# Kernel tuning notes

Measured on AMD Instinct MI355X. Metric: run time of the kernel, lower is better.

The kernel has to match this reference:

```python
import jax, jax.numpy as jnp
import numpy as np

N_NODES = 50000
N_EDGES = 800000
NFEAT, NHID, NHEAD, NCLASS = 512, 64, 8, 40
NEG_SLOPE = 0.2  # LeakyReLU alpha from __init__


def setup_inputs() -> dict:
    key = jax.random.key(0)
    ks = jax.random.split(key, 8)
    glorot = lambda k, shape: jax.random.normal(k, shape, jnp.float32) * (2.0 / (shape[-2] + shape[-1])) ** 0.5
    return {
        "x": jax.random.normal(ks[0], (N_NODES, NFEAT), jnp.float32),
        "edge_list": jax.random.randint(ks[1], (2, N_EDGES), 0, N_NODES, jnp.int32),
        # nhead input-layer GATconv params: weight [H, nfeat, nhid], att [H, 2*nhid], bias [H, nhid]
        "W1": glorot(ks[2], (NHEAD, NFEAT, NHID)),
        "a1": jax.random.normal(ks[3], (NHEAD, 2 * NHID), jnp.float32) * 0.1,
        "b1": jnp.zeros((NHEAD, NHID), jnp.float32),
        # single output-head GATconv: [nhid*nhead, nclass]
        "W2": glorot(ks[4], (NHEAD * NHID, NCLASS)),
        "a2": jax.random.normal(ks[5], (2 * NCLASS,), jnp.float32) * 0.1,
        "b2": jnp.zeros((NCLASS,), jnp.float32),
    }


def _gat_layer(x, W, a, b, src, dst, n_nodes):
    """One GATconv head (eval mode, dropout = identity)."""
    h = x @ W                                  # [N, F]
    f = W.shape[-1]
    s_src = h @ a[:f]                          # [N] per-node src score
    s_dst = h @ a[f:]                          # [N] per-node dst score
    e = jax.nn.leaky_relu(s_src[src] + s_dst[dst], NEG_SLOPE)  # [E]
    # segment softmax over incoming edges of each dst node (numerically stable)
    m = jax.ops.segment_max(e, dst, num_segments=n_nodes)
    m = jax.lax.stop_gradient(jnp.where(jnp.isfinite(m), m, 0.0))
    w = jnp.exp(e - m[dst])
    denom = jax.ops.segment_sum(w, dst, num_segments=n_nodes)
    alpha = w / jnp.maximum(denom[dst], 1e-16)                 # [E]
    out = jax.ops.segment_sum(alpha[:, None] * h[src], dst, num_segments=n_nodes)
    return out + b


def reference(x, edge_list, W1, a1, b1, W2, a2, b2):
    n = x.shape[0]
    src, dst = edge_list[0], edge_list[1]
    # multi-head input layer, concat along feature dim
    heads = jax.vmap(lambda W, a, b: _gat_layer(x, W, a, b, src, dst, n))(W1, a1, b1)  # [H, N, nhid]
    h = jax.nn.elu(jnp.transpose(heads, (1, 0, 2)).reshape(n, -1))                      # [N, H*nhid]
    # single output head (mean over nhead_out=1)
    out = _gat_layer(h, W2, a2, b2, src, dst, n)                                        # [N, nclass]
    return jax.nn.log_softmax(out, axis=1)
```

## Files before the change

kernel.cpp:

```cpp
#include <hip/hip_runtime.h>
#include <math.h>

#define N_NODES 50000
#define N_EDGES 800000
#define NFEAT 512
#define NHID 64
#define NHEAD 8
#define NCLASS 40
#define NEG_SLOPE 0.2f

#define N_RT 3125
#define N_RT_PAD 3128
#define SCAN_NBLK 49
#define RT_BLK 4
#define ATT1_CHUNK 12500

typedef __attribute__((ext_vector_type(8))) short short8;
typedef __attribute__((ext_vector_type(4))) short short4v;
typedef __attribute__((ext_vector_type(4))) float f32x4;

__device__ __forceinline__ float bf2f(short s) {
    return __uint_as_float(((unsigned)(unsigned short)s) << 16);
}
__device__ __forceinline__ short f2bf(float f) {
    unsigned u = __float_as_uint(f);
    unsigned r = (u + 0x7FFFu + ((u >> 16) & 1u)) >> 16;
    return (short)(unsigned short)r;
}
__device__ __forceinline__ int swz(int s) { return s ^ ((s >> 4) & 7); }



__global__ void count_deg(const int* __restrict__ el, int* __restrict__ deg) {
    int e = blockIdx.x * blockDim.x + threadIdx.x;
    if (e < N_EDGES) atomicAdd(&deg[el[N_EDGES + e]], 1);
}

__global__ __launch_bounds__(256) void scan1(const int* __restrict__ deg,
                                             int* __restrict__ loc,
                                             int* __restrict__ bsum) {
    int tid = threadIdx.x, lane = tid & 63, w = tid >> 6;
    int base = blockIdx.x * 1024 + tid * 4;
    int d0 = (base + 0 < N_NODES) ? deg[base + 0] : 0;
    int d1 = (base + 1 < N_NODES) ? deg[base + 1] : 0;
    int d2 = (base + 2 < N_NODES) ? deg[base + 2] : 0;
    int d3 = (base + 3 < N_NODES) ? deg[base + 3] : 0;
    int s0 = d0, s1 = s0 + d1, s2 = s1 + d2, s3 = s2 + d3;
    int t = s3;
#pragma unroll
    for (int d = 1; d < 64; d <<= 1) {
        int u = __shfl_up(t, d);
        if (lane >= d) t += u;
    }
    __shared__ int wsum[4];
    if (lane == 63) wsum[w] = t;
    __syncthreads();
    int woff = 0;
#pragma unroll
    for (int j = 0; j < 4; ++j) woff += (j < w) ? wsum[j] : 0;
    int excl = woff + t - s3;
    if (base + 0 < N_NODES) loc[base + 0] = excl + s0;
    if (base + 1 < N_NODES) loc[base + 1] = excl + s1;
    if (base + 2 < N_NODES) loc[base + 2] = excl + s2;
    if (base + 3 < N_NODES) loc[base + 3] = excl + s3;
    if (tid == 255) bsum[blockIdx.x] = woff + t;
}

__global__ __launch_bounds__(256) void scan3(const int* __restrict__ deg,
                                             const int* __restrict__ loc,
                                             const int* __restrict__ bsum,
                                             int* __restrict__ ptr,
                                             int* __restrict__ cursor) {
    __shared__ int sOff;
    if (threadIdx.x < 64) {
        int lane = threadIdx.x;
        int v = (lane < SCAN_NBLK && lane < (int)blockIdx.x) ? bsum[lane] : 0;
#pragma unroll
        for (int m = 1; m < 64; m <<= 1) v += __shfl_xor(v, m);
        if (lane == 0) sOff = v;
    }
    __syncthreads();
    int off = sOff;
    int base = blockIdx.x * 1024 + threadIdx.x * 4;
    if (blockIdx.x == 0 && threadIdx.x == 0) ptr[0] = 0;
#pragma unroll
    for (int k = 0; k < 4; ++k) {
        int i = base + k;
        if (i < N_NODES) {
            int P = off + loc[i];
            ptr[i + 1] = P;
            cursor[i] = P - deg[i];
        }
    }
}

__global__ void scatter_k(const int* __restrict__ el, int* __restrict__ cursor,
                          int* __restrict__ esrc) {
    int e = blockIdx.x * blockDim.x + threadIdx.x;
    if (e >= N_EDGES) return;
    int dst = el[N_EDGES + e];
    int p = atomicAdd(&cursor[dst], 1);
    esrc[p] = el[e];
}

__global__ __launch_bounds__(256) void pack_w(const float* __restrict__ W1,
                                              const float* __restrict__ W2,
                                              const float* __restrict__ a1,
                                              short* __restrict__ Wp1a,
                                              short* __restrict__ Wp2) {
    int t = blockIdx.x * 256 + threadIdx.x;
    if (t < 36864) {
        int l = t & 63;
        int idx = t >> 6;
        int ct = idx % 9;
        int ksg = idx / 9;
        int ks = ksg & 15, g = ksg >> 4;
        short8 o;
        if (ct < 8) {
            int c = g * 128 + ct * 16 + (l & 15);
            int head = c >> 6, f = c & 63;
            int k0 = ks * 32 + (l >> 4) * 8;
#pragma unroll
            for (int j = 0; j < 8; ++j)
                o[j] = f2bf(W1[(size_t)head * NFEAT * NHID + (k0 + j) * NHID + f]);
        } else {
            int col = l & 15;
            int k0 = ks * 32 + (l >> 4) * 8;
#pragma unroll
            for (int j = 0; j < 8; ++j) o[j] = 0;
            if (col < 4) {
                int head = 2 * g + (col >> 1);
                const float* av = a1 + head * 128 + (col & 1) * 64;
                const float* wb = W1 + (size_t)head * NFEAT * NHID;
#pragma unroll
                for (int j = 0; j < 8; ++j) {
                    const float* wr = wb + (size_t)(k0 + j) * NHID;
                    float s = 0.f;
                    for (int f = 0; f < NHID; ++f) s += wr[f] * av[f];
                    o[j] = f2bf(s);
                }
            }
        }
        *(short8*)(Wp1a + (size_t)t * 8) = o;
    } else if (t < 36864 + 3072) {
        int u = t - 36864;
        int l = u & 63;
        int kc = u >> 6;
        int ct2 = kc % 3, ks = kc / 3;
        int col = ct2 * 16 + (l & 15);
        short8 o;
#pragma unroll
        for (int j = 0; j < 8; ++j) {
            int kp = ks * 32 + (l >> 4) * 8 + j;
            int head = kp >> 6, fp = kp & 63;
            int l15 = fp >> 2, ctp = fp & 3;
            int ct = ((head & 1) << 2) | ctp;
            int gg = head >> 1;
            int orig_k = gg * 128 + ct * 16 + l15;
            o[j] = (col < NCLASS) ? f2bf(W2[(size_t)orig_k * NCLASS + col]) : (short)0;
        }
        *(short8*)(Wp2 + (size_t)u * 8) = o;
    }
}

__global__ __launch_bounds__(256, 2) void gemm1(const float* __restrict__ x,
                                                const short* __restrict__ Wp1a,
                                                short* __restrict__ h1p,
                                                float* __restrict__ s1s,
                                                float* __restrict__ s1d) {
    __shared__ short As[RT_BLK * 16 * 64 * 8];
    int w = threadIdx.x >> 6, l = threadIdx.x & 63;
    int g = w;
    int rt0 = blockIdx.x * RT_BLK;
    int row0 = rt0 * 16;

#pragma unroll
    for (int u = 0; u < 4 * RT_BLK; ++u) {
        int idx = threadIdx.x + u * 256;
        int rl = idx >> 6, cg = idx & 63;
        int row = row0 + rl;
        short8 o;
        if (row < N_NODES) {
            const float* p = x + (size_t)row * NFEAT + cg * 8;
            f32x4 v0 = __builtin_nontemporal_load((const f32x4*)p);
            f32x4 v1 = __builtin_nontemporal_load((const f32x4*)(p + 4));
            o[0] = f2bf(v0[0]); o[1] = f2bf(v0[1]); o[2] = f2bf(v0[2]); o[3] = f2bf(v0[3]);
            o[4] = f2bf(v1[0]); o[5] = f2bf(v1[1]); o[6] = f2bf(v1[2]); o[7] = f2bf(v1[3]);
        } else {
#pragma unroll
            for (int j = 0; j < 8; ++j) o[j] = 0;
        }
        int rtl = rl >> 4, rloc = rl & 15, ks = cg >> 2, sub = cg & 3;
        int slot = (rtl * 16 + ks) * 64 + rloc + sub * 16;
        *(short8*)(As + swz(slot) * 8) = o;
    }
    __syncthreads();

    f32x4 acc[RT_BLK][9];
#pragma unroll
    for (int i = 0; i < RT_BLK; ++i)
#pragma unroll
        for (int ct = 0; ct < 9; ++ct) acc[i][ct] = (f32x4){0.f, 0.f, 0.f, 0.f};

    const short* bP = Wp1a + (size_t)g * (16 * 9 * 512) + l * 8;
#pragma unroll 2
    for (int ks = 0; ks < 16; ++ks) {
        short8 b[9];
#pragma unroll
        for (int ct = 0; ct < 9; ++ct) b[ct] = *(const short8*)(bP + ks * 4608 + ct * 512);
        short8 a[RT_BLK];
#pragma unroll
        for (int i = 0; i < RT_BLK; ++i)
            a[i] = *(const short8*)(As + swz((i * 16 + ks) * 64 + l) * 8);
#pragma unroll
        for (int i = 0; i < RT_BLK; ++i)
#pragma unroll
            for (int ct = 0; ct < 9; ++ct)
                acc[i][ct] = __builtin_amdgcn_mfma_f32_16x16x32_bf16(a[i], b[ct], acc[i][ct], 0, 0, 0);
    }

    int l15 = l & 15;
    int rbase = (l >> 4) * 4;
#pragma unroll
    for (int i = 0; i < RT_BLK; ++i)
#pragma unroll
        for (int r = 0; r < 4; ++r) {
            int row = (rt0 + i) * 16 + rbase + r;
            if (row < N_NODES) {
                short4v o0, o1;
#pragma unroll
                for (int c = 0; c < 4; ++c) { o0[c] = f2bf(acc[i][c][r]); o1[c] = f2bf(acc[i][4 + c][r]); }
                size_t base = (size_t)row * 512 + g * 128 + l15 * 4;
                *(short4v*)(h1p + base) = o0;
                *(short4v*)(h1p + base + 64) = o1;
                float sv = acc[i][8][r];
                if (l15 == 0)      s1s[row * 8 + 2 * g]     = sv;
                else if (l15 == 1) s1d[row * 8 + 2 * g]     = sv;
                else if (l15 == 2) s1s[row * 8 + 2 * g + 1] = sv;
                else if (l15 == 3) s1d[row * 8 + 2 * g + 1] = sv;
            }
        }
}

__global__ __launch_bounds__(256, 4) void att1(const int* __restrict__ ptr,
                                               const int* __restrict__ esrc,
                                               const float* __restrict__ s1s,
                                               const float* __restrict__ s1d,
                                               const short* __restrict__ h1p,
                                               const float* __restrict__ b1,
                                               short* __restrict__ hcat,
                                               int n0) {
    int n = n0 + blockIdx.x * 4 + (threadIdx.x >> 6);
    int l = threadIdx.x & 63;
    if (n >= N_NODES) return;
    int beg = ptr[n], end = ptr[n + 1];
    int h = l >> 3;
    float sd = s1d[n * 8 + h];
    float den = 0.f;
    float acc[8] = {0.f, 0.f, 0.f, 0.f, 0.f, 0.f, 0.f, 0.f};
    const short* hb = h1p + l * 8;
    if (beg < end) {
        int last = end - 1;
        int p1 = (beg + 1 <= last) ? beg + 1 : last;
        int p2 = (beg + 2 <= last) ? beg + 2 : last;
        int p3 = (beg + 3 <= last) ? beg + 3 : last;
        int s0 = esrc[beg], s1 = esrc[p1], s2 = esrc[p2], s3 = esrc[p3];
        short8 v0 = *(const short8*)(hb + (size_t)s0 * 512);
        short8 v1 = *(const short8*)(hb + (size_t)s1 * 512);
        short8 v2 = *(const short8*)(hb + (size_t)s2 * 512);
        short8 v3 = *(const short8*)(hb + (size_t)s3 * 512);
        float ss0 = s1s[s0 * 8 + h], ss1 = s1s[s1 * 8 + h];
        float ss2 = s1s[s2 * 8 + h], ss3 = s1s[s3 * 8 + h];
        for (int i = beg; i < end; i += 4) {
            int ni = i + 4;
            int t0 = s0, t1 = s1, t2 = s2, t3 = s3;
            short8 u0 = v0, u1 = v1, u2 = v2, u3 = v3;
            float ts0 = ss0, ts1 = ss1, ts2 = ss2, ts3 = ss3;
            if (ni < end) {
                int q1 = (ni + 1 <= last) ? ni + 1 : last;
                int q2 = (ni + 2 <= last) ? ni + 2 : last;
                int q3 = (ni + 3 <= last) ? ni + 3 : last;
                t0 = esrc[ni]; t1 = esrc[q1]; t2 = esrc[q2]; t3 = esrc[q3];
                u0 = *(const short8*)(hb + (size_t)t0 * 512);
                u1 = *(const short8*)(hb + (size_t)t1 * 512);
                u2 = *(const short8*)(hb + (size_t)t2 * 512);
                u3 = *(const short8*)(hb + (size_t)t3 * 512);
                ts0 = s1s[t0 * 8 + h]; ts1 = s1s[t1 * 8 + h];
                ts2 = s1s[t2 * 8 + h]; ts3 = s1s[t3 * 8 + h];
            }
            float e0 = ss0 + sd, e1 = ss1 + sd, e2 = ss2 + sd, e3 = ss3 + sd;
            e0 = fmaxf(e0, NEG_SLOPE * e0);
            e1 = fmaxf(e1, NEG_SLOPE * e1);
            e2 = fmaxf(e2, NEG_SLOPE * e2);
            e3 = fmaxf(e3, NEG_SLOPE * e3);
            float w0 = __expf(e0);
            float w1 = (i + 1 < end) ? __expf(e1) : 0.f;
            float w2 = (i + 2 < end) ? __expf(e2) : 0.f;
            float w3 = (i + 3 < end) ? __expf(e3) : 0.f;
            den += (w0 + w1) + (w2 + w3);
#pragma unroll
            for (int j = 0; j < 8; ++j)
                acc[j] += (w0 * bf2f(v0[j]) + w1 * bf2f(v1[j])) +
                          (w2 * bf2f(v2[j]) + w3 * bf2f(v3[j]));
            s0 = t0; s1 = t1; s2 = t2; s3 = t3;
            v0 = u0; v1 = u1; v2 = u2; v3 = u3;
            ss0 = ts0; ss1 = ts1; ss2 = ts2; ss3 = ts3;
        }
    }
    float rden = 1.f / fmaxf(den, 1e-16f);
    short8 o;
#pragma unroll
    for (int j = 0; j < 8; ++j) {
        int forig = (j & 3) * 16 + (l & 7) * 2 + (j >> 2);
        float v = acc[j] * rden + b1[h * 64 + forig];
        v = v > 0.f ? v : (__expf(v) - 1.f);
        o[j] = f2bf(v);
    }
    *(short8*)(hcat + (size_t)n * 512 + l * 8) = o;
}

__global__ __launch_bounds__(256) void gemm2(const short* __restrict__ hcat,
                                             const short* __restrict__ Wp2,
                                             const float* __restrict__ a2,
                                             short* __restrict__ h2,
                                             float* __restrict__ s2s,
                                             float* __restrict__ s2d) {
    int w = threadIdx.x >> 6, l = threadIdx.x & 63;
    int rt = blockIdx.x * 4 + w;
    int arow = rt * 16 + (l & 15);
    const short* aBase = hcat + (size_t)arow * 512 + (l >> 4) * 8;
    f32x4 acc[3];
#pragma unroll
    for (int ct = 0; ct < 3; ++ct) acc[ct] = (f32x4){0.f, 0.f, 0.f, 0.f};
#pragma unroll 2
    for (int ks = 0; ks < 16; ++ks) {
        short8 a = *(const short8*)(aBase + ks * 32);
        const short* bp = Wp2 + (size_t)(ks * 3) * 512 + l * 8;
#pragma unroll
        for (int ct = 0; ct < 3; ++ct) {
            short8 b = *(const short8*)(bp + ct * 512);
            acc[ct] = __builtin_amdgcn_mfma_f32_16x16x32_bf16(a, b, acc[ct], 0, 0, 0);
        }
    }
    float ps[4] = {0.f, 0.f, 0.f, 0.f}, pd[4] = {0.f, 0.f, 0.f, 0.f};
    int cl = l & 15, rb = (l >> 4) * 4;
#pragma unroll
    for (int ct = 0; ct < 3; ++ct) {
        int col = ct * 16 + cl;
        if (col < NCLASS) {
#pragma unroll
            for (int r = 0; r < 4; ++r) {
                ps[r] += acc[ct][r] * a2[col];
                pd[r] += acc[ct][r] * a2[NCLASS + col];
                int row = rt * 16 + rb + r;
                if (row < N_NODES) h2[(size_t)row * NCLASS + col] = f2bf(acc[ct][r]);
            }
        }
    }
#pragma unroll
    for (int mask = 1; mask < 16; mask <<= 1)
#pragma unroll
        for (int r = 0; r < 4; ++r) {
            ps[r] += __shfl_xor(ps[r], mask);
            pd[r] += __shfl_xor(pd[r], mask);
        }
    if (cl == 0) {
#pragma unroll
        for (int r = 0; r < 4; ++r) {
            int row = rt * 16 + rb + r;
            if (row < N_NODES) { s2s[row] = ps[r]; s2d[row] = pd[r]; }
        }
    }
}

__global__ __launch_bounds__(256, 4) void att2(const int* __restrict__ ptr,
                                               const int* __restrict__ esrc,
                                               const float* __restrict__ s2s,
                                               const float* __restrict__ s2d,
                                               const short* __restrict__ h2,
                                               const float* __restrict__ b2,
                                               float* __restrict__ out) {
    int n = blockIdx.x * 4 + (threadIdx.x >> 6);
    int l = threadIdx.x & 63;
    if (n >= N_NODES) return;
    int beg = ptr[n], end = ptr[n + 1];
    float sd = s2d[n];
    float den = 0.f, acc = 0.f;
    int last = end - 1;
    bool act = (l < NCLASS);
    for (int i = beg; i < end; i += 4) {
        int i1 = (i + 1 <= last) ? i + 1 : last;
        int i2 = (i + 2 <= last) ? i + 2 : last;
        int i3 = (i + 3 <= last) ? i + 3 : last;
        int s0 = esrc[i], s1 = esrc[i1], s2 = esrc[i2], s3 = esrc[i3];
        float h0 = act ? bf2f(h2[(size_t)s0 * NCLASS + l]) : 0.f;
        float h1 = act ? bf2f(h2[(size_t)s1 * NCLASS + l]) : 0.f;
        float hh2 = act ? bf2f(h2[(size_t)s2 * NCLASS + l]) : 0.f;
        float h3 = act ? bf2f(h2[(size_t)s3 * NCLASS + l]) : 0.f;
        float e0 = s2s[s0] + sd;
        float e1 = s2s[s1] + sd;
        float e2 = s2s[s2] + sd;
        float e3 = s2s[s3] + sd;
        e0 = fmaxf(e0, NEG_SLOPE * e0);
        e1 = fmaxf(e1, NEG_SLOPE * e1);
        e2 = fmaxf(e2, NEG_SLOPE * e2);
        e3 = fmaxf(e3, NEG_SLOPE * e3);
        float w0 = __expf(e0);
        float w1 = (i + 1 < end) ? __expf(e1) : 0.f;
        float w2 = (i + 2 < end) ? __expf(e2) : 0.f;
        float w3 = (i + 3 < end) ? __expf(e3) : 0.f;
        den += (w0 + w1) + (w2 + w3);
        acc += (w0 * h0 + w1 * h1) + (w2 * hh2 + w3 * h3);
    }
    float v = act ? acc / fmaxf(den, 1e-16f) + b2[l] : -INFINITY;
    float mx = v;
#pragma unroll
    for (int o = 32; o; o >>= 1) mx = fmaxf(mx, __shfl_down(mx, o));
    mx = __shfl(mx, 0);
    float ex = act ? __expf(v - mx) : 0.f;
    float s = ex;
#pragma unroll
    for (int o = 32; o; o >>= 1) s += __shfl_down(s, o);
    s = __shfl(s, 0);
    float ls = __logf(s);
    if (act) out[(size_t)n * NCLASS + l] = v - mx - ls;
}


extern "C" void kernel_launch(void* const* d_in, const int* in_sizes, int n_in,
                              void* d_out, int out_size, void* d_ws, size_t ws_size,
                              hipStream_t stream) {
    const float* x  = (const float*)d_in[0];
    const int*   el = (const int*)d_in[1];
    const float* W1 = (const float*)d_in[2];
    const float* a1 = (const float*)d_in[3];
    const float* b1 = (const float*)d_in[4];
    const float* W2 = (const float*)d_in[5];
    const float* a2 = (const float*)d_in[6];
    const float* b2 = (const float*)d_in[7];
    float* out = (float*)d_out;

    short* sbase = (short*)d_ws;
    short* Wp1a  = sbase;
    short* hcat  = sbase + 25624576;
    short* h1p   = sbase + 51249152;
    short* Wp2   = sbase + 77111296;
    short* h2    = sbase + 77135872;
    float* fbase = (float*)(sbase + 79135872);
    float* s1s   = fbase;
    float* s1d   = fbase + 400000;
    float* s2s   = fbase + 800000;
    float* s2d   = fbase + 850000;
    int*   ibase = (int*)(fbase + 900000);
    int*   deg    = ibase;
    int*   ptr    = ibase + 50000;
    int*   cursor = ibase + 100001;
    int*   esrc   = ibase + 150001;
    int*   loc    = ibase + 950001;
    int*   bsum   = ibase + 1000001;

    hipMemsetAsync(deg, 0, (size_t)N_NODES * 4, stream);
    count_deg<<<(N_EDGES + 255) / 256, 256, 0, stream>>>(el, deg);
    scan1<<<SCAN_NBLK, 256, 0, stream>>>(deg, loc, bsum);
    scan3<<<SCAN_NBLK, 256, 0, stream>>>(deg, loc, bsum, ptr, cursor);
    scatter_k<<<(N_EDGES + 255) / 256, 256, 0, stream>>>(el, cursor, esrc);

    pack_w<<<156, 256, 0, stream>>>(W1, W2, a1, Wp1a, Wp2);

    gemm1<<<N_RT_PAD / RT_BLK, 256, 0, stream>>>(x, Wp1a, h1p, s1s, s1d);
    att1<<<ATT1_CHUNK / 4, 256, 0, stream>>>(ptr, esrc, s1s, s1d, h1p, b1, hcat, 0);
    att1<<<ATT1_CHUNK / 4, 256, 0, stream>>>(ptr, esrc, s1s, s1d, h1p, b1, hcat, 12500);
    att1<<<ATT1_CHUNK / 4, 256, 0, stream>>>(ptr, esrc, s1s, s1d, h1p, b1, hcat, 25000);
    att1<<<ATT1_CHUNK / 4, 256, 0, stream>>>(ptr, esrc, s1s, s1d, h1p, b1, hcat, 37500);

    gemm2<<<N_RT_PAD / 4, 256, 0, stream>>>(hcat, Wp2, a2, h2, s2s, s2d);
    att2<<<(N_NODES + 3) / 4, 256, 0, stream>>>(ptr, esrc, s2s, s2d, h2, b2, out);
}
```

Measured before the change: 524.2 us.

## Pad layer-2 features to 64 columns and process four edges per wavefront in att2

gemm2 now writes h2 into a 64-column padded buffer (h2p) placed in an unused region of the workspace. att2 splits each wavefront into four 16-lane groups; each group handles one edge and each lane loads four bf16 values in a single vector load. Partial sums are combined across groups with xor shuffles, and the log-softmax reduction now runs within 16 lanes. This raises memory-level parallelism and cuts per-edge instruction count in the second attention pass, at the cost of larger h2 storage and extra padding writes.

```diff
diff --git a/kernel.cpp b/kernel.cpp
--- a/kernel.cpp
+++ b/kernel.cpp
@@ -322,7 +322,7 @@
 __global__ __launch_bounds__(256) void gemm2(const short* __restrict__ hcat,
                                              const short* __restrict__ Wp2,
                                              const float* __restrict__ a2,
-                                             short* __restrict__ h2,
+                                             short* __restrict__ h2p,
                                              float* __restrict__ s2s,
                                              float* __restrict__ s2d) {
     int w = threadIdx.x >> 6, l = threadIdx.x & 63;
@@ -347,13 +347,16 @@
 #pragma unroll
     for (int ct = 0; ct < 3; ++ct) {
         int col = ct * 16 + cl;
+#pragma unroll
+        for (int r = 0; r < 4; ++r) {
+            int row = rt * 16 + rb + r;
+            if (row < N_NODES) h2p[(size_t)row * 64 + col] = f2bf(acc[ct][r]);
+        }
         if (col < NCLASS) {
 #pragma unroll
             for (int r = 0; r < 4; ++r) {
                 ps[r] += acc[ct][r] * a2[col];
                 pd[r] += acc[ct][r] * a2[NCLASS + col];
-                int row = rt * 16 + rb + r;
-                if (row < N_NODES) h2[(size_t)row * NCLASS + col] = f2bf(acc[ct][r]);
             }
         }
     }
@@ -377,7 +380,7 @@
                                                const int* __restrict__ esrc,
                                                const float* __restrict__ s2s,
                                                const float* __restrict__ s2d,
-                                               const short* __restrict__ h2,
+                                               const short* __restrict__ h2p,
                                                const float* __restrict__ b2,
                                                float* __restrict__ out) {
     int n = blockIdx.x * 4 + (threadIdx.x >> 6);
@@ -385,45 +388,63 @@
     if (n >= N_NODES) return;
     int beg = ptr[n], end = ptr[n + 1];
     float sd = s2d[n];
-    float den = 0.f, acc = 0.f;
-    int last = end - 1;
-    bool act = (l < NCLASS);
-    for (int i = beg; i < end; i += 4) {
-        int i1 = (i + 1 <= last) ? i + 1 : last;
-        int i2 = (i + 2 <= last) ? i + 2 : last;
-        int i3 = (i + 3 <= last) ? i + 3 : last;
-        int s0 = esrc[i], s1 = esrc[i1], s2 = esrc[i2], s3 = esrc[i3];
-        float h0 = act ? bf2f(h2[(size_t)s0 * NCLASS + l]) : 0.f;
-        float h1 = act ? bf2f(h2[(size_t)s1 * NCLASS + l]) : 0.f;
-        float hh2 = act ? bf2f(h2[(size_t)s2 * NCLASS + l]) : 0.f;
-        float h3 = act ? bf2f(h2[(size_t)s3 * NCLASS + l]) : 0.f;
-        float e0 = s2s[s0] + sd;
-        float e1 = s2s[s1] + sd;
-        float e2 = s2s[s2] + sd;
-        float e3 = s2s[s3] + sd;
-        e0 = fmaxf(e0, NEG_SLOPE * e0);
-        e1 = fmaxf(e1, NEG_SLOPE * e1);
-        e2 = fmaxf(e2, NEG_SLOPE * e2);
-        e3 = fmaxf(e3, NEG_SLOPE * e3);
-        float w0 = __expf(e0);
-        float w1 = (i + 1 < end) ? __expf(e1) : 0.f;
-        float w2 = (i + 2 < end) ? __expf(e2) : 0.f;
-        float w3 = (i + 3 < end) ? __expf(e3) : 0.f;
-        den += (w0 + w1) + (w2 + w3);
-        acc += (w0 * h0 + w1 * h1) + (w2 * hh2 + w3 * h3);
-    }
-    float v = act ? acc / fmaxf(den, 1e-16f) + b2[l] : -INFINITY;
-    float mx = v;
-#pragma unroll
-    for (int o = 32; o; o >>= 1) mx = fmaxf(mx, __shfl_down(mx, o));
-    mx = __shfl(mx, 0);
-    float ex = act ? __expf(v - mx) : 0.f;
-    float s = ex;
-#pragma unroll
-    for (int o = 32; o; o >>= 1) s += __shfl_down(s, o);
-    s = __shfl(s, 0);
+    int grp = l >> 4, cl = l & 15;
+    bool act16 = cl < 10;
+    float den = 0.f, a0 = 0.f, a1 = 0.f, a2v = 0.f, a3 = 0.f;
+    if (beg < end) {
+        int last = end - 1;
+        for (int i = beg; i < end; i += 4) {
+            int e = i + grp;
+            bool valid = e < end;
+            int src = esrc[valid ? e : last];
+            float sc = s2s[src] + sd;
+            sc = fmaxf(sc, NEG_SLOPE * sc);
+            float wgt = valid ? __expf(sc) : 0.f;
+            short4v hv = *(const short4v*)(h2p + (size_t)src * 64 + cl * 4);
+            den += wgt;
+            if (act16) {
+                a0 += wgt * bf2f(hv[0]);
+                a1 += wgt * bf2f(hv[1]);
+                a2v += wgt * bf2f(hv[2]);
+                a3 += wgt * bf2f(hv[3]);
+            }
+        }
+    }
+#pragma unroll
+    for (int m = 16; m < 64; m <<= 1) {
+        den += __shfl_xor(den, m);
+        a0  += __shfl_xor(a0, m);
+        a1  += __shfl_xor(a1, m);
+        a2v += __shfl_xor(a2v, m);
+        a3  += __shfl_xor(a3, m);
+    }
+    float rden = 1.f / fmaxf(den, 1e-16f);
+    float v0, v1, v2, v3;
+    if (act16) {
+        int c0 = cl * 4;
+        v0 = a0 * rden + b2[c0 + 0];
+        v1 = a1 * rden + b2[c0 + 1];
+        v2 = a2v * rden + b2[c0 + 2];
+        v3 = a3 * rden + b2[c0 + 3];
+    } else { v0 = v1 = v2 = v3 = -INFINITY; }
+    float mx = fmaxf(fmaxf(v0, v1), fmaxf(v2, v3));
+#pragma unroll
+    for (int m = 1; m < 16; m <<= 1) mx = fmaxf(mx, __shfl_xor(mx, m));
+    float e0 = act16 ? __expf(v0 - mx) : 0.f;
+    float e1 = act16 ? __expf(v1 - mx) : 0.f;
+    float e2 = act16 ? __expf(v2 - mx) : 0.f;
+    float e3 = act16 ? __expf(v3 - mx) : 0.f;
+    float s = (e0 + e1) + (e2 + e3);
+#pragma unroll
+    for (int m = 1; m < 16; m <<= 1) s += __shfl_xor(s, m);
     float ls = __logf(s);
-    if (act) out[(size_t)n * NCLASS + l] = v - mx - ls;
+    if (l < 16 && act16) {
+        int c0 = cl * 4;
+        out[(size_t)n * NCLASS + c0 + 0] = v0 - mx - ls;
+        out[(size_t)n * NCLASS + c0 + 1] = v1 - mx - ls;
+        out[(size_t)n * NCLASS + c0 + 2] = v2 - mx - ls;
+        out[(size_t)n * NCLASS + c0 + 3] = v3 - mx - ls;
+    }
 }
 
 
@@ -442,10 +463,10 @@
 
     short* sbase = (short*)d_ws;
     short* Wp1a  = sbase;
+    short* h2p   = sbase + 4000000;
     short* hcat  = sbase + 25624576;
     short* h1p   = sbase + 51249152;
     short* Wp2   = sbase + 77111296;
-    short* h2    = sbase + 77135872;
     float* fbase = (float*)(sbase + 79135872);
     float* s1s   = fbase;
     float* s1d   = fbase + 400000;
@@ -473,6 +494,6 @@
     att1<<<ATT1_CHUNK / 4, 256, 0, stream>>>(ptr, esrc, s1s, s1d, h1p, b1, hcat, 25000);
     att1<<<ATT1_CHUNK / 4, 256, 0, stream>>>(ptr, esrc, s1s, s1d, h1p, b1, hcat, 37500);
 
-    gemm2<<<N_RT_PAD / 4, 256, 0, stream>>>(hcat, Wp2, a2, h2, s2s, s2d);
-    att2<<<(N_NODES + 3) / 4, 256, 0, stream>>>(ptr, esrc, s2s, s2d, h2, b2, out);
-}
+    gemm2<<<N_RT_PAD / 4, 256, 0, stream>>>(hcat, Wp2, a2, h2p, s2s, s2d);
+    att2<<<(N_NODES + 3) / 4, 256, 0, stream>>>(ptr, esrc, s2s, s2d, h2p, b2, out);
+}
```

Measured after the change: 497.9 us. 5.0% less time.
